# Performance work log

Hardware: AMD Instinct MI355X
Metric: run time of the kernel (lower is better)

Reference implementation:

```python
import jax, jax.numpy as jnp
import numpy as np


def setup_inputs() -> dict:
    key = jax.random.key(0)
    k1, k2 = jax.random.split(key)
    B, L, J, N = 8, 32, 128, 512
    ypred = jax.random.normal(k1, (B, L, J, N), dtype=jnp.float32)
    xyz = jax.random.normal(k2, (B, L, N, 3), dtype=jnp.float32)
    return {"ypred": ypred, "xyz": xyz}


def _pairwise_dist(x):
    # x: [BL, N, 3] -> Euclidean distance [BL, N, N] via the mm trick,
    # with the diagonal forced to exactly 0 (matching torch.cdist(x, x)).
    sq = jnp.sum(x * x, axis=-1)                       # [BL, N]
    d2 = sq[:, :, None] + sq[:, None, :] - 2.0 * jnp.einsum('bnd,bmd->bnm', x, x)
    d2 = jnp.maximum(d2, 0.0)
    dist = jnp.sqrt(d2)
    n = x.shape[1]
    eye = jnp.eye(n, dtype=bool)
    return jnp.where(eye[None, :, :], 0.0, dist)


def reference(ypred, xyz):
    B, L, J, N = ypred.shape
    x = xyz.reshape(B * L, N, 3)
    dist = _pairwise_dist(x)                           # [BL, N, N]
    max_idx = jnp.argmax(dist, axis=2)                 # [BL, N] farthest point
    dist_masked = jnp.where(dist == 0.0, 1e6, dist)    # mask self (and exact dupes)
    min_idx = jnp.argmin(dist_masked, axis=2)          # [BL, N] nearest point

    # per-point logit vectors: [BL, N, J]
    yp = jnp.transpose(ypred, (0, 1, 3, 2)).reshape(B * L, N, J)
    sim = jnp.einsum('bnj,bmj->bnm', yp, yp)           # [BL, N, N]

    sim_at_max = jnp.take_along_axis(sim, max_idx[:, :, None], axis=2)[..., 0]
    sim_at_min = jnp.take_along_axis(sim, min_idx[:, :, None], axis=2)[..., 0]
    return jnp.mean(sim_at_max - sim_at_min)
```

## Files before the change

### kernel.cpp

```cpp
#include <hip/hip_runtime.h>

#pragma clang fp contract(off)

#define NBATCH 256
#define NPTS   512
#define JDIM   128
#define NPAIR  (NBATCH * NPTS)

__global__ __launch_bounds__(512) void argmm_kernel(
    const float* __restrict__ xyz,
    int* __restrict__ pmax,
    int* __restrict__ pmin)
{
    __shared__ float4 xyzS[NPTS + 4];

    const int t  = threadIdx.x;
    const int bl = blockIdx.x >> 2;
    const int qq = blockIdx.x & 3;
    const float* xp = xyz + (size_t)bl * NPTS * 3;

    {
        float x = xp[3 * t], y = xp[3 * t + 1], z = xp[3 * t + 2];
        float sq = (x * x + y * y) + z * z;
        xyzS[t + (t >> 7)] = make_float4(-2.0f * x, -2.0f * y, -2.0f * z, sq);
    }
    __syncthreads();

    const int p = qq * 128 + (t >> 2);
    const int q = t & 3;

    float4 ov = xyzS[p + (p >> 7)];
    float ox = -0.5f * ov.x, oy = -0.5f * ov.y, oz = -0.5f * ov.z;
    float oq_ = ov.w;

    const float4* xb = &xyzS[q];
    const int m0 = q << 7;
    float bmax = -1.0f, bmin = 3.0e38f;
    int   ima  = m0,    imi  = m0;
    #pragma unroll 8
    for (int mm = 0; mm < 128; ++mm) {
        int m = m0 + mm;
        float4 qv = xb[m];
        float dt = (ox * qv.x + oy * qv.y) + oz * qv.z;
        float d2 = (oq_ + qv.w) + dt;
        bool gt = d2 > bmax;
        ima = gt ? m : ima;  bmax = gt ? d2 : bmax;
        bool lt = (d2 < bmin) && (d2 > 0.0f);
        imi = lt ? m : imi;  bmin = lt ? d2 : bmin;
    }

    #pragma unroll
    for (int st = 1; st <= 2; st <<= 1) {
        float obmax = __shfl_xor(bmax, st); int oima = __shfl_xor(ima, st);
        float obmin = __shfl_xor(bmin, st); int oimi = __shfl_xor(imi, st);
        bool hi = (t & st) != 0;
        float lmax = hi ? obmax : bmax;  int lima = hi ? oima : ima;
        float hmax = hi ? bmax : obmax;  int hima = hi ? ima  : oima;
        bool w = hmax > lmax;
        bmax = w ? hmax : lmax;  ima = w ? hima : lima;
        float lmin = hi ? obmin : bmin;  int limi = hi ? oimi : imi;
        float hmin = hi ? bmin : obmin;  int himi = hi ? imi  : oimi;
        bool x2 = hmin < lmin;
        bmin = x2 ? hmin : lmin;  imi = x2 ? himi : limi;
    }

    if (q == 0)      pmax[bl * NPTS + p] = ima;
    else if (q == 1) pmin[bl * NPTS + p] = imi;
}

__global__ __launch_bounds__(512) void sim_kernel(
    const float* __restrict__ ypred,
    const int* __restrict__ pmax,
    const int* __restrict__ pmin,
    float* __restrict__ partials)
{
    __shared__ float L[16 * NPTS];
    __shared__ float wred[8];

    const int t  = threadIdx.x;
    const int bl = blockIdx.x >> 3;
    const int c  = blockIdx.x & 7;

    const int pma = pmax[bl * NPTS + t];
    const int pmi = pmin[bl * NPTS + t];

    const float4* src = (const float4*)(ypred + (size_t)bl * JDIM * NPTS
                                              + (size_t)c * 16 * NPTS);
    float4 v0 = src[t], v1 = src[512 + t], v2 = src[1024 + t], v3 = src[1536 + t];
    float4* dst = (float4*)L;
    dst[t] = v0;  dst[512 + t] = v1;  dst[1024 + t] = v2;  dst[1536 + t] = v3;
    __syncthreads();

    float accP = 0.0f, accM = 0.0f;
    #pragma unroll
    for (int r = 0; r < 16; ++r) {
        float a  = L[r * NPTS + t];
        float b  = L[r * NPTS + pma];
        float cm = L[r * NPTS + pmi];
        accP = fmaf(a, b, accP);
        accM = fmaf(a, cm, accM);
    }

    float d = accP - accM;
    #pragma unroll
    for (int off = 32; off > 0; off >>= 1)
        d += __shfl_down(d, off);
    if ((t & 63) == 0) wred[t >> 6] = d;
    __syncthreads();
    if (t == 0) {
        float ssum = 0.0f;
        #pragma unroll
        for (int w = 0; w < 8; ++w) ssum += wred[w];
        partials[blockIdx.x] = ssum;
    }
}

__global__ __launch_bounds__(1024) void reduce_mean_kernel(
    const float* __restrict__ partials, float* __restrict__ out)
{
    const int t = threadIdx.x;
    float v = partials[t] + partials[t + 1024];
    #pragma unroll
    for (int off = 32; off > 0; off >>= 1)
        v += __shfl_down(v, off);

    __shared__ float w[16];
    if ((t & 63) == 0) w[t >> 6] = v;
    __syncthreads();
    if (t == 0) {
        float s = 0.0f;
        #pragma unroll
        for (int i = 0; i < 16; ++i) s += w[i];
        out[0] = s * (1.0f / (float)NPAIR);
    }
}

extern "C" void kernel_launch(void* const* d_in, const int* in_sizes, int n_in,
                              void* d_out, int out_size, void* d_ws, size_t ws_size,
                              hipStream_t stream) {
    const float* ypred = (const float*)d_in[0];
    const float* xyz   = (const float*)d_in[1];

    int*   pmax     = (int*)d_ws;
    int*   pmin     = pmax + NPAIR;
    float* partials = (float*)(pmin + NPAIR);
    float* out      = (float*)d_out;

    argmm_kernel<<<4 * NBATCH, 512, 0, stream>>>(xyz, pmax, pmin);
    sim_kernel<<<8 * NBATCH, 512, 0, stream>>>(ypred, pmax, pmin, partials);
    reduce_mean_kernel<<<1, 1024, 0, stream>>>(partials, out);
}
```

Baseline: 116.8 us.

## Pack distance math with v_pk ops and load ypred directly to LDS

The argmax/argmin kernel now stores the point coordinates in a structure-of-arrays LDS layout. It evaluates two candidate distances per iteration using packed FP32 multiply/add inline assembly, and reads the query point straight from global memory. The sim kernel replaces its register-staged global-to-LDS copy with global_load_lds 16-byte direct loads, issued before the index loads, followed by an explicit vmcnt wait. This is meant to cut VALU instruction count and register traffic, at the cost of relying on hardware-specific builtins and per-wave LDS addressing semantics.

```diff
diff --git a/kernel.cpp b/kernel.cpp
--- a/kernel.cpp
+++ b/kernel.cpp
@@ -7,12 +7,20 @@
 #define JDIM   128
 #define NPAIR  (NBATCH * NPTS)
 
+typedef float f32x2 __attribute__((ext_vector_type(2)));
+
+__device__ __forceinline__ void gload_lds16(const void* g, void* l) {
+    __builtin_amdgcn_global_load_lds(
+        (const __attribute__((address_space(1))) void*)g,
+        (__attribute__((address_space(3))) void*)l, 16, 0, 0);
+}
+
 __global__ __launch_bounds__(512) void argmm_kernel(
     const float* __restrict__ xyz,
     int* __restrict__ pmax,
     int* __restrict__ pmin)
 {
-    __shared__ float4 xyzS[NPTS + 4];
+    __shared__ f32x2 soa[4 * 260 + 4];
 
     const int t  = threadIdx.x;
     const int bl = blockIdx.x >> 2;
@@ -22,31 +30,54 @@
     {
         float x = xp[3 * t], y = xp[3 * t + 1], z = xp[3 * t + 2];
         float sq = (x * x + y * y) + z * z;
-        xyzS[t + (t >> 7)] = make_float4(-2.0f * x, -2.0f * y, -2.0f * z, sq);
+        int q = t >> 7, j = (t & 127) >> 1, hf = t & 1;
+        float* b = (float*)&soa[q * 260 + j];
+        b[hf]       = -2.0f * x;
+        b[128 + hf] = -2.0f * y;
+        b[256 + hf] = -2.0f * z;
+        b[384 + hf] = sq;
     }
-    __syncthreads();
 
     const int p = qq * 128 + (t >> 2);
     const int q = t & 3;
+    float ox = xp[3 * p], oy = xp[3 * p + 1], oz = xp[3 * p + 2];
+    float oq = (ox * ox + oy * oy) + oz * oz;
+    __syncthreads();
 
-    float4 ov = xyzS[p + (p >> 7)];
-    float ox = -0.5f * ov.x, oy = -0.5f * ov.y, oz = -0.5f * ov.z;
-    float oq_ = ov.w;
+    const f32x2 ox2 = {ox, ox}, oy2 = {oy, oy}, oz2 = {oz, oz}, oq2 = {oq, oq};
+    const f32x2* Xp = &soa[q * 260 +   0];
+    const f32x2* Yp = &soa[q * 260 +  64];
+    const f32x2* Zp = &soa[q * 260 + 128];
+    const f32x2* Wp = &soa[q * 260 + 192];
 
-    const float4* xb = &xyzS[q];
     const int m0 = q << 7;
     float bmax = -1.0f, bmin = 3.0e38f;
     int   ima  = m0,    imi  = m0;
     #pragma unroll 8
-    for (int mm = 0; mm < 128; ++mm) {
-        int m = m0 + mm;
-        float4 qv = xb[m];
-        float dt = (ox * qv.x + oy * qv.y) + oz * qv.z;
-        float d2 = (oq_ + qv.w) + dt;
-        bool gt = d2 > bmax;
-        ima = gt ? m : ima;  bmax = gt ? d2 : bmax;
-        bool lt = (d2 < bmin) && (d2 > 0.0f);
-        imi = lt ? m : imi;  bmin = lt ? d2 : bmin;
+    for (int j = 0; j < 64; ++j) {
+        f32x2 px = Xp[j], py = Yp[j], pz = Zp[j], pw = Wp[j];
+        f32x2 t1, t2, t3, s, dt, da, d2;
+        asm("v_pk_mul_f32 %0, %1, %2" : "=v"(t1) : "v"(ox2), "v"(px));
+        asm("v_pk_mul_f32 %0, %1, %2" : "=v"(t2) : "v"(oy2), "v"(py));
+        asm("v_pk_add_f32 %0, %1, %2" : "=v"(s)  : "v"(t1),  "v"(t2));
+        asm("v_pk_mul_f32 %0, %1, %2" : "=v"(t3) : "v"(oz2), "v"(pz));
+        asm("v_pk_add_f32 %0, %1, %2" : "=v"(dt) : "v"(s),   "v"(t3));
+        asm("v_pk_add_f32 %0, %1, %2" : "=v"(da) : "v"(oq2), "v"(pw));
+        asm("v_pk_add_f32 %0, %1, %2" : "=v"(d2) : "v"(da),  "v"(dt));
+
+        const int m = m0 + 2 * j;
+        {
+            float d = d2.x;
+            bool gt = d > bmax;  ima = gt ? m : ima;  bmax = gt ? d : bmax;
+            bool lt = (d < bmin) && (d > 0.0f);
+            imi = lt ? m : imi;  bmin = lt ? d : bmin;
+        }
+        {
+            float d = d2.y;  const int m1 = m + 1;
+            bool gt = d > bmax;  ima = gt ? m1 : ima;  bmax = gt ? d : bmax;
+            bool lt = (d < bmin) && (d > 0.0f);
+            imi = lt ? m1 : imi; bmin = lt ? d : bmin;
+        }
     }
 
     #pragma unroll
@@ -74,21 +105,24 @@
     const int* __restrict__ pmin,
     float* __restrict__ partials)
 {
-    __shared__ float L[16 * NPTS];
+    __shared__ __align__(16) float L[16 * NPTS];
     __shared__ float wred[8];
 
     const int t  = threadIdx.x;
     const int bl = blockIdx.x >> 3;
     const int c  = blockIdx.x & 7;
+    const int wbase = t & ~63;
+
+    const float4* src = (const float4*)(ypred + (size_t)bl * JDIM * NPTS
+                                              + (size_t)c * 16 * NPTS);
+    #pragma unroll
+    for (int qd = 0; qd < 4; ++qd)
+        gload_lds16(src + qd * 512 + t, (float4*)L + qd * 512 + wbase);
 
     const int pma = pmax[bl * NPTS + t];
     const int pmi = pmin[bl * NPTS + t];
 
-    const float4* src = (const float4*)(ypred + (size_t)bl * JDIM * NPTS
-                                              + (size_t)c * 16 * NPTS);
-    float4 v0 = src[t], v1 = src[512 + t], v2 = src[1024 + t], v3 = src[1536 + t];
-    float4* dst = (float4*)L;
-    dst[t] = v0;  dst[512 + t] = v1;  dst[1024 + t] = v2;  dst[1536 + t] = v3;
+    asm volatile("s_waitcnt vmcnt(0)" ::: "memory");
     __syncthreads();
 
     float accP = 0.0f, accM = 0.0f;
```

New measurement: 119.4 us. 1.02x slower.

## Double-buffer sim kernel with direct global-to-LDS loads across four chunks

Applied to the files above, without the earlier changes.

The similarity kernel now runs a quarter as many blocks, and each block walks four 16-row chunks of the logits. Rows are loaded straight into two LDS buffers with global_load_lds, using vmcnt waits and barriers so the next chunk streams in while the current one is computed. The goal is to hide global-load latency and skip the register round trip when staging the memory-bound ypred stream. In exchange, per-block LDS doubles, which may reduce occupancy, and fewer blocks means less parallelism to cover latency.

```diff
diff --git a/kernel.cpp b/kernel.cpp
--- a/kernel.cpp
+++ b/kernel.cpp
@@ -6,6 +6,12 @@
 #define NPTS   512
 #define JDIM   128
 #define NPAIR  (NBATCH * NPTS)
+
+__device__ __forceinline__ void gload_lds16(const void* g, void* l) {
+    __builtin_amdgcn_global_load_lds(
+        (const __attribute__((address_space(1))) void*)g,
+        (__attribute__((address_space(3))) void*)l, 16, 0, 0);
+}
 
 __global__ __launch_bounds__(512) void argmm_kernel(
     const float* __restrict__ xyz,
@@ -74,44 +80,65 @@
     const int* __restrict__ pmin,
     float* __restrict__ partials)
 {
-    __shared__ float L[16 * NPTS];
+    __shared__ __align__(16) float Lt[2][16 * NPTS];
     __shared__ float wred[8];
 
     const int t  = threadIdx.x;
-    const int bl = blockIdx.x >> 3;
-    const int c  = blockIdx.x & 7;
+    const int bl = blockIdx.x >> 1;
+    const int h  = blockIdx.x & 1;
+    const int wbase = t & ~63;
+
+    const float4* src = (const float4*)(ypred + (size_t)bl * JDIM * NPTS
+                                              + (size_t)h * 4 * 16 * NPTS);
 
     const int pma = pmax[bl * NPTS + t];
     const int pmi = pmin[bl * NPTS + t];
 
-    const float4* src = (const float4*)(ypred + (size_t)bl * JDIM * NPTS
-                                              + (size_t)c * 16 * NPTS);
-    float4 v0 = src[t], v1 = src[512 + t], v2 = src[1024 + t], v3 = src[1536 + t];
-    float4* dst = (float4*)L;
-    dst[t] = v0;  dst[512 + t] = v1;  dst[1024 + t] = v2;  dst[1536 + t] = v3;
-    __syncthreads();
+    #pragma unroll
+    for (int qd = 0; qd < 4; ++qd)
+        gload_lds16(src + qd * 512 + t, (float4*)Lt[0] + qd * 512 + wbase);
+    #pragma unroll
+    for (int qd = 0; qd < 4; ++qd)
+        gload_lds16(src + 2048 + qd * 512 + t,
+                    (float4*)Lt[1] + qd * 512 + wbase);
 
-    float accP = 0.0f, accM = 0.0f;
     #pragma unroll
-    for (int r = 0; r < 16; ++r) {
-        float a  = L[r * NPTS + t];
-        float b  = L[r * NPTS + pma];
-        float cm = L[r * NPTS + pmi];
-        accP = fmaf(a, b, accP);
-        accM = fmaf(a, cm, accM);
-    }
+    for (int i = 0; i < 4; ++i) {
+        if (i < 3) asm volatile("s_waitcnt vmcnt(4)" ::: "memory");
+        else       asm volatile("s_waitcnt vmcnt(0)" ::: "memory");
+        __builtin_amdgcn_s_barrier();
 
-    float d = accP - accM;
-    #pragma unroll
-    for (int off = 32; off > 0; off >>= 1)
-        d += __shfl_down(d, off);
-    if ((t & 63) == 0) wred[t >> 6] = d;
-    __syncthreads();
-    if (t == 0) {
-        float ssum = 0.0f;
+        const float* L = Lt[i & 1];
+        float accP = 0.0f, accM = 0.0f;
         #pragma unroll
-        for (int w = 0; w < 8; ++w) ssum += wred[w];
-        partials[blockIdx.x] = ssum;
+        for (int r = 0; r < 16; ++r) {
+            float a  = L[r * NPTS + t];
+            float b  = L[r * NPTS + pma];
+            float cm = L[r * NPTS + pmi];
+            accP = fmaf(a, b, accP);
+            accM = fmaf(a, cm, accM);
+        }
+        float d = accP - accM;
+        #pragma unroll
+        for (int off = 32; off > 0; off >>= 1)
+            d += __shfl_down(d, off);
+        if ((t & 63) == 0) wred[t >> 6] = d;
+
+        asm volatile("s_waitcnt lgkmcnt(0)" ::: "memory");
+        __builtin_amdgcn_s_barrier();
+
+        if (i + 2 < 4) {
+            #pragma unroll
+            for (int qd = 0; qd < 4; ++qd)
+                gload_lds16(src + (i + 2) * 2048 + qd * 512 + t,
+                            (float4*)Lt[i & 1] + qd * 512 + wbase);
+        }
+        if (t == 0) {
+            float ssum = 0.0f;
+            #pragma unroll
+            for (int w = 0; w < 8; ++w) ssum += wred[w];
+            partials[bl * 8 + h * 4 + i] = ssum;
+        }
     }
 }
 
@@ -147,6 +174,6 @@
     float* out      = (float*)d_out;
 
     argmm_kernel<<<4 * NBATCH, 512, 0, stream>>>(xyz, pmax, pmin);
-    sim_kernel<<<8 * NBATCH, 512, 0, stream>>>(ypred, pmax, pmin, partials);
+    sim_kernel<<<2 * NBATCH, 512, 0, stream>>>(ypred, pmax, pmin, partials);
     reduce_mean_kernel<<<1, 1024, 0, stream>>>(partials, out);
 }
```

Measured after the change: 119.1 us. 2.0% more time.
